# Performance work log

Hardware: AMD Instinct MI355X
Metric: run time of the kernel (lower is better)

## Reference

```python
import jax, jax.numpy as jnp
import numpy as np

N, E, F, D, EH, G, L, NG = 50000, 800000, 32, 32, 96, 128, 3, 500


def setup_inputs() -> dict:
    key = jax.random.key(0)
    ks = iter(jax.random.split(key, 32))
    w = lambda shape: jax.random.normal(next(ks), shape, dtype=jnp.float32) * 0.05
    inp = {
        "node_features": jax.random.normal(next(ks), (N, F), dtype=jnp.float32),
        "enc_W": w((F, D)), "enc_b": w((D,)),
        "msg_W1": w((L, 2 * D, EH)), "msg_b1": w((L, EH)),
        "msg_W2": w((L, EH, EH)), "msg_b2": w((L, EH)),
        "rmsg_W1": w((L, 2 * D, EH)), "rmsg_b1": w((L, EH)),
        "rmsg_W2": w((L, EH, EH)), "rmsg_b2": w((L, EH)),
        "gru_Wih": w((L, 3 * D, EH)), "gru_Whh": w((L, 3 * D, D)),
        "gru_bih": w((L, 3 * D)), "gru_bhh": w((L, 3 * D)),
        "agg_W1": w((D, 2 * G)), "agg_b1": w((2 * G,)),
        "agg_W2": w((G, G)), "agg_b2": w((G,)),
        "from_idx": jax.random.randint(next(ks), (E,), 0, N),
        "to_idx": jax.random.randint(next(ks), (E,), 0, N),
        "graph_idx": jnp.sort(jax.random.randint(next(ks), (N,), 0, NG)),
        "n_graphs": NG,
    }
    return inp


def _mlp(x, W1, b1, W2, b2):
    # Linear -> ReLU -> Linear (message net)
    return jax.nn.relu(x @ W1 + b1) @ W2 + b2


def _gru_step(x, h, Wih, Whh, bih, bhh):
    # torch nn.GRU single-step, gate order r, z, n
    gi = x @ Wih.T + bih  # [n, 3D]
    gh = h @ Whh.T + bhh  # [n, 3D]
    ir, iz, inn = jnp.split(gi, 3, axis=-1)
    hr, hz, hn = jnp.split(gh, 3, axis=-1)
    r = jax.nn.sigmoid(ir + hr)
    z = jax.nn.sigmoid(iz + hz)
    n = jnp.tanh(inn + r * hn)
    return (1.0 - z) * n + z * h


def _forward(node_features, enc_W, enc_b, msg_W1, msg_b1, msg_W2, msg_b2,
             rmsg_W1, rmsg_b1, rmsg_W2, rmsg_b2, gru_Wih, gru_Whh, gru_bih, gru_bhh,
             agg_W1, agg_b1, agg_W2, agg_b2, from_idx, to_idx, graph_idx, n_graphs):
    # GraphEncoder: single Linear
    h = node_features @ enc_W + enc_b  # [N, D]
    n_nodes = h.shape[0]
    n_layers = msg_W1.shape[0]
    for l in range(n_layers):  # small fixed layer count
        fs = h[from_idx]  # [E, D] gather
        ts = h[to_idx]    # [E, D] gather
        # forward-direction messages: gather -> concat -> MLP -> scatter_add to to_idx
        m = _mlp(jnp.concatenate([fs, ts], axis=-1), msg_W1[l], msg_b1[l], msg_W2[l], msg_b2[l])
        agg = jax.ops.segment_sum(m, to_idx, num_segments=n_nodes)
        # reverse direction: roles of from/to swapped, scatter to from_idx
        mr = _mlp(jnp.concatenate([ts, fs], axis=-1), rmsg_W1[l], rmsg_b1[l], rmsg_W2[l], rmsg_b2[l])
        agg = agg + jax.ops.segment_sum(mr, from_idx, num_segments=n_nodes)
        # node update via GRU (aggregated messages as input, node states as hidden)
        h = _gru_step(agg, h, gru_Wih[l], gru_Whh[l], gru_bih[l], gru_bhh[l])
    # GraphAggregator: gated node transform + scatter_add by graph, then Linear
    g = h @ agg_W1 + agg_b1  # [N, 2G]
    gdim = agg_W2.shape[0]
    gated = jax.nn.sigmoid(g[:, :gdim]) * g[:, gdim:]
    graph_states = jax.ops.segment_sum(gated, graph_idx, num_segments=n_graphs)  # [n_graphs, G]
    return graph_states @ agg_W2 + agg_b2


def reference(node_features, enc_W, enc_b, msg_W1, msg_b1, msg_W2, msg_b2,
              rmsg_W1, rmsg_b1, rmsg_W2, rmsg_b2, gru_Wih, gru_Whh, gru_bih, gru_bhh,
              agg_W1, agg_b1, agg_W2, agg_b2, from_idx, to_idx, graph_idx, n_graphs):
    return _forward(node_features, enc_W, enc_b, msg_W1, msg_b1, msg_W2, msg_b2,
                    rmsg_W1, rmsg_b1, rmsg_W2, rmsg_b2, gru_Wih, gru_Whh, gru_bih, gru_bhh,
                    agg_W1, agg_b1, agg_W2, agg_b2, from_idx, to_idx, graph_idx, n_graphs)
```

## Files before the change

### kernel.cpp

```cpp
#include <hip/hip_runtime.h>

#define SB 512

typedef __attribute__((ext_vector_type(8))) short short8;
typedef __attribute__((ext_vector_type(4))) float f32x4;

__device__ inline unsigned short f2bf(float f) {
    unsigned u = __float_as_uint(f);
    unsigned r = (u + 0x7fffu + ((u >> 16) & 1u)) >> 16;
    return (unsigned short)r;
}
__device__ inline unsigned pack2bf(float x, float y) {
    return (unsigned)f2bf(x) | ((unsigned)f2bf(y) << 16);
}

__global__ void count_rank_kernel(const int* __restrict__ from_idx, const int* __restrict__ to_idx,
                                  int* __restrict__ cnt_to, int* __restrict__ cnt_from,
                                  int* __restrict__ rank_to, int* __restrict__ rank_from, int E) {
    int e = blockIdx.x * blockDim.x + threadIdx.x;
    if (e >= E) return;
    int f = from_idx[e], t = to_idx[e];
    rank_to[e] = atomicAdd(&cnt_to[t], 1);
    rank_from[e] = atomicAdd(&cnt_from[f], 1);
}

__global__ void __launch_bounds__(SB) scanA_kernel(const int* __restrict__ cnt_to,
                                                   const int* __restrict__ cnt_from,
                                                   int* __restrict__ bsum, int nblk, int N) {
    const int* cnt = blockIdx.y ? cnt_from : cnt_to;
    __shared__ int s[SB];
    int tid = threadIdx.x;
    int i = blockIdx.x * SB + tid;
    s[tid] = (i < N) ? cnt[i] : 0;
    __syncthreads();
    for (int d = SB / 2; d > 0; d >>= 1) {
        if (tid < d) s[tid] += s[tid + d];
        __syncthreads();
    }
    if (tid == 0) bsum[blockIdx.y * nblk + blockIdx.x] = s[0];
}

__global__ void scanB_kernel(int* __restrict__ bsum, int* __restrict__ bbase,
                             int* __restrict__ off_to, int* __restrict__ off_from,
                             int nblk, int N) {
    int tid = threadIdx.x;
    if (tid < 2) {
        const int* bs = bsum + tid * nblk;
        int* bb = bbase + tid * nblk;
        int run = 0;
        for (int i = 0; i < nblk; ++i) { bb[i] = run; run += bs[i]; }
        if (tid == 0) off_to[N] = run; else off_from[N] = run;
    }
}

__global__ void __launch_bounds__(SB) scanC_kernel(const int* __restrict__ cnt_to,
                                                   const int* __restrict__ cnt_from,
                                                   const int* __restrict__ bbase,
                                                   int* __restrict__ off_to, int* __restrict__ off_from,
                                                   int nblk, int N) {
    const int* cnt = blockIdx.y ? cnt_from : cnt_to;
    int* off = blockIdx.y ? off_from : off_to;
    __shared__ int s[SB];
    int tid = threadIdx.x;
    int i = blockIdx.x * SB + tid;
    int v = (i < N) ? cnt[i] : 0;
    s[tid] = v;
    __syncthreads();
    for (int d = 1; d < SB; d <<= 1) {
        int t = s[tid];
        int add = (tid >= d) ? s[tid - d] : 0;
        __syncthreads();
        s[tid] = t + add;
        __syncthreads();
    }
    if (i < N) off[i] = s[tid] - v + bbase[blockIdx.y * nblk + blockIdx.x];
}

__global__ void fill_kernel(const int* __restrict__ from_idx, const int* __restrict__ to_idx,
                            const int* __restrict__ off_to, const int* __restrict__ off_from,
                            const int* __restrict__ rank_to, const int* __restrict__ rank_from,
                            int* __restrict__ list_to, int* __restrict__ list_from, int E) {
    int e = blockIdx.x * blockDim.x + threadIdx.x;
    if (e >= E) return;
    int f = from_idx[e], t = to_idx[e];
    list_to[off_to[t] + rank_to[e]] = f;
    list_from[off_from[f] + rank_from[e]] = t;
}

__global__ void compose_kernel(const float* __restrict__ W2, const float* __restrict__ rW2,
                               const float* __restrict__ Wih,
                               const float* __restrict__ b2, const float* __restrict__ rb2,
                               float* __restrict__ M1, float* __restrict__ M2,
                               float* __restrict__ v12) {
    int l = blockIdx.x / 97, j = blockIdx.x % 97;
    int k = threadIdx.x;
    const float* wih = Wih + l * 9216 + k * 96;
    if (j < 96) {
        const float* w2  = W2 + l * 9216 + j * 96;
        const float* rw2 = rW2 + l * 9216 + j * 96;
        float a1 = 0.f, a2 = 0.f;
        for (int m = 0; m < 96; ++m) {
            float wv = wih[m];
            a1 = fmaf(w2[m], wv, a1);
            a2 = fmaf(rw2[m], wv, a2);
        }
        M1[l * 9216 + j * 96 + k] = a1;
        M2[l * 9216 + j * 96 + k] = a2;
    } else {
        const float* bb = b2 + l * 96;
        const float* rbb = rb2 + l * 96;
        float a1 = 0.f, a2 = 0.f;
        for (int m = 0; m < 96; ++m) {
            float wv = wih[m];
            a1 = fmaf(bb[m], wv, a1);
            a2 = fmaf(rbb[m], wv, a2);
        }
        v12[l * 192 + k] = a1;
        v12[l * 192 + 96 + k] = a2;
    }
}

__global__ void repack_kernel(const float* __restrict__ M1, const float* __restrict__ M2,
                              const float* __restrict__ Whh,
                              const float* __restrict__ W1f, const float* __restrict__ W1r,
                              unsigned* __restrict__ M1bc, unsigned* __restrict__ M2bc,
                              unsigned* __restrict__ Whhbc, unsigned* __restrict__ W1bc) {
    int idx = blockIdx.x * 256 + threadIdx.x;
    if (idx < 13824) {
        int l = idx / 4608, r = idx % 4608, c = r / 48, wd = r % 48;
        const float* src = M1 + l * 9216;
        M1bc[idx] = pack2bf(src[(2 * wd) * 96 + c], src[(2 * wd + 1) * 96 + c]);
    } else if (idx < 27648) {
        int j = idx - 13824;
        int l = j / 4608, r = j % 4608, c = r / 48, wd = r % 48;
        const float* src = M2 + l * 9216;
        M2bc[j] = pack2bf(src[(2 * wd) * 96 + c], src[(2 * wd + 1) * 96 + c]);
    } else if (idx < 32256) {
        int j = idx - 27648;
        int l = j / 1536, r = j % 1536, c = r / 16, wd = r % 16;
        const float* src = Whh + l * 3072 + c * 32;
        Whhbc[j] = pack2bf(src[2 * wd], src[2 * wd + 1]);
    } else if (idx < 32256 + 18432) {
        int j = idx - 32256;
        int l = j / 6144, r = j % 6144, C = r / 16, wd = r % 16;
        const float* src; int col, rb;
        if (C < 96)       { src = W1f + l * 6144; col = C;       rb = 0;  }
        else if (C < 192) { src = W1f + l * 6144; col = C - 96;  rb = 32; }
        else if (C < 288) { src = W1r + l * 6144; col = C - 192; rb = 0;  }
        else              { src = W1r + l * 6144; col = C - 288; rb = 32; }
        W1bc[j] = pack2bf(src[(rb + 2 * wd) * 96 + col], src[(rb + 2 * wd + 1) * 96 + col]);
    }
}

__global__ void __launch_bounds__(256) enc_gemm(const float* __restrict__ IN,
                                                const float* __restrict__ W, const float* __restrict__ bias,
                                                float* __restrict__ OUT, unsigned short* __restrict__ hb16, int N) {
    __shared__ float tile[64][33];
    int n0 = blockIdx.x * 64, tid = threadIdx.x;
    for (int idx = tid; idx < 64 * 32; idx += 256) {
        int r = idx >> 5, c = idx & 31;
        int n = n0 + r;
        tile[r][c] = (n < N) ? IN[(long)n * 32 + c] : 0.f;
    }
    __syncthreads();
    int lane = tid & 63;
    int w = __builtin_amdgcn_readfirstlane(tid >> 6);
    float acc[8] = {0};
    const float* Wp = W + w * 8;
#pragma unroll 4
    for (int j = 0; j < 32; ++j) {
        float a = tile[lane][j];
#pragma unroll
        for (int c = 0; c < 8; ++c) acc[c] = fmaf(a, Wp[j * 32 + c], acc[c]);
    }
    int n = n0 + lane;
    if (n >= N) return;
    float* outp = OUT + (long)n * 32 + w * 8;
    unsigned short* bp = hb16 + (long)n * 32 + w * 8;
#pragma unroll
    for (int c = 0; c < 8; ++c) {
        float v = acc[c] + bias[w * 8 + c];
        outp[c] = v;
        bp[c] = f2bf(v);
    }
}

__global__ void __launch_bounds__(512) proj_mfma(
    const unsigned* __restrict__ hb, const unsigned* __restrict__ W1bc,
    const float* __restrict__ b1f, const float* __restrict__ b1r,
    unsigned short* __restrict__ PaF16, unsigned short* __restrict__ PbF16,
    unsigned short* __restrict__ PaR16, unsigned short* __restrict__ PbR16, int N)
{
    int tid = threadIdx.x;
    int lane = tid & 63;
    int w = __builtin_amdgcn_readfirstlane(tid >> 6);
    int nt = w >> 1, cg = w & 1;
    int kgrp = lane >> 4, l15 = lane & 15;
    int ntile = blockIdx.x * 64 + nt * 16;
    int arow = ntile + l15;
    long arc = (arow < N) ? arow : (N - 1);
    short8 a = *(const short8*)(hb + arc * 16 + kgrp * 4);

    unsigned short* Pa16 = cg ? PaR16 : PaF16;
    unsigned short* Pb16 = cg ? PbR16 : PbF16;
    const float* b1 = cg ? b1r : b1f;

    f32x4 acc[12];
#pragma unroll
    for (int ct = 0; ct < 12; ++ct) {
        int col = cg * 192 + ct * 16 + l15;
        short8 b = *(const short8*)(W1bc + (long)col * 16 + kgrp * 4);
        acc[ct] = __builtin_amdgcn_mfma_f32_16x16x32_bf16(a, b, (f32x4){0.f,0.f,0.f,0.f}, 0, 0, 0);
    }
    int nbase = ntile + kgrp * 4;
#pragma unroll
    for (int ct = 0; ct < 6; ++ct) {
        int col = ct * 16 + l15;
#pragma unroll
        for (int i = 0; i < 4; ++i) {
            int n = nbase + i;
            if (n < N) Pa16[(long)n * 96 + col] = f2bf(acc[ct][i]);
        }
    }
#pragma unroll
    for (int ct = 6; ct < 12; ++ct) {
        int col = (ct - 6) * 16 + l15;
        float bv = b1[col];
#pragma unroll
        for (int i = 0; i < 4; ++i) {
            int n = nbase + i;
            if (n < N) Pb16[(long)n * 96 + col] = f2bf(acc[ct][i] + bv);
        }
    }
}

__global__ void __launch_bounds__(256) agg_bf16(
    const int* __restrict__ offF, const int* __restrict__ listF,
    const int* __restrict__ offR, const int* __restrict__ listR,
    const unsigned* __restrict__ PaF, const unsigned* __restrict__ PaR,
    const unsigned short* __restrict__ PbF16, const unsigned short* __restrict__ PbR16,
    unsigned* __restrict__ AFb, unsigned* __restrict__ ARb, int N)
{
    const int* off; const int* list; const unsigned* Pa; const unsigned short* Pb16; unsigned* AB;
    if (blockIdx.y == 0) { off = offF; list = listF; Pa = PaF; Pb16 = PbF16; AB = AFb; }
    else                 { off = offR; list = listR; Pa = PaR; Pb16 = PbR16; AB = ARb; }
    int n = __builtin_amdgcn_readfirstlane((blockIdx.x * 256 + threadIdx.x) >> 6);
    int lane = threadIdx.x & 63;
    if (n >= N) return;
    int li = (lane < 48) ? lane : 47;
    bool act = lane < 48;
    float sx = 0.f, sy = 0.f;
    if (act) {
        unsigned s = *(const unsigned*)(Pb16 + (long)n * 96 + 2 * li);
        sx = __uint_as_float(s << 16);
        sy = __uint_as_float(s & 0xffff0000u);
    }
    float a0 = 0.f, a1 = 0.f;
    int beg = off[n], end = off[n + 1];
    if (end > beg) {
        int nb = (end - beg + 7) >> 3;
        for (int b = 0; b < nb; ++b) {
            int base = beg + b * 8;
            unsigned u[8]; float m[8];
#pragma unroll
            for (int q = 0; q < 8; ++q) {
                int idx = base + q;
                bool v = idx < end;
                int src = list[v ? idx : end - 1];
                u[q] = Pa[(long)src * 48 + li];
                m[q] = v ? 1.f : 0.f;
            }
#pragma unroll
            for (int q = 0; q < 8; ++q) {
                a0 += m[q] * fmaxf(__uint_as_float(u[q] << 16) + sx, 0.f);
                a1 += m[q] * fmaxf(__uint_as_float(u[q] & 0xffff0000u) + sy, 0.f);
            }
        }
    }
    if (act) AB[(long)n * 48 + li] = pack2bf(a0, a1);
}

__global__ void __launch_bounds__(512) gru3_kernel(
    const unsigned* __restrict__ AFb, const unsigned* __restrict__ ARb,
    const unsigned* __restrict__ M1bc, const unsigned* __restrict__ M2bc,
    const unsigned* __restrict__ Whhbc,
    const float* __restrict__ v12,
    const int* __restrict__ offF, const int* __restrict__ offR,
    const float* __restrict__ h, const unsigned* __restrict__ hb,
    const float* __restrict__ bih, const float* __restrict__ bhh,
    float* __restrict__ hout, unsigned short* __restrict__ hbout, int N)
{
    int tid = threadIdx.x;
    int lane = tid & 63;
    int w = __builtin_amdgcn_readfirstlane(tid >> 6);
    int nt = w >> 1, cg = w & 1;
    int kgrp = lane >> 4;
    int c = cg * 16 + (lane & 15);
    int ntile = blockIdx.x * 64 + nt * 16;
    int arow = ntile + (lane & 15);
    long arc = (arow < N) ? arow : (N - 1);

    f32x4 acc[3]; f32x4 gh[3];
#pragma unroll
    for (int g = 0; g < 3; ++g) { acc[g] = (f32x4){0.f,0.f,0.f,0.f}; gh[g] = (f32x4){0.f,0.f,0.f,0.f}; }

    const unsigned* afp = AFb + arc * 48 + kgrp * 4;
    const unsigned* arp = ARb + arc * 48 + kgrp * 4;
#pragma unroll
    for (int k0 = 0; k0 < 3; ++k0) {
        short8 a = *(const short8*)(afp + k0 * 16);
#pragma unroll
        for (int g = 0; g < 3; ++g) {
            int col = g * 32 + c;
            short8 b = *(const short8*)(M1bc + (long)col * 48 + k0 * 16 + kgrp * 4);
            acc[g] = __builtin_amdgcn_mfma_f32_16x16x32_bf16(a, b, acc[g], 0, 0, 0);
        }
    }
#pragma unroll
    for (int k0 = 0; k0 < 3; ++k0) {
        short8 a = *(const short8*)(arp + k0 * 16);
#pragma unroll
        for (int g = 0; g < 3; ++g) {
            int col = g * 32 + c;
            short8 b = *(const short8*)(M2bc + (long)col * 48 + k0 * 16 + kgrp * 4);
            acc[g] = __builtin_amdgcn_mfma_f32_16x16x32_bf16(a, b, acc[g], 0, 0, 0);
        }
    }
    {
        short8 ha = *(const short8*)(hb + arc * 16 + kgrp * 4);
#pragma unroll
        for (int g = 0; g < 3; ++g) {
            int col = g * 32 + c;
            short8 b = *(const short8*)(Whhbc + (long)col * 16 + kgrp * 4);
            gh[g] = __builtin_amdgcn_mfma_f32_16x16x32_bf16(ha, b, gh[g], 0, 0, 0);
        }
    }

    float v1r[3], v2r[3], bihv[3], bhhv[3];
#pragma unroll
    for (int g = 0; g < 3; ++g) {
        int col = g * 32 + c;
        v1r[g] = v12[col]; v2r[g] = v12[96 + col];
        bihv[g] = bih[col]; bhhv[g] = bhh[col];
    }
    int nbase = ntile + kgrp * 4;
#pragma unroll
    for (int i = 0; i < 4; ++i) {
        int n = nbase + i;
        if (n < N) {
            float dF = (float)(offF[n + 1] - offF[n]);
            float dR = (float)(offR[n + 1] - offR[n]);
            float gir = acc[0][i] + dF * v1r[0] + dR * v2r[0] + bihv[0];
            float giz = acc[1][i] + dF * v1r[1] + dR * v2r[1] + bihv[1];
            float gin = acc[2][i] + dF * v1r[2] + dR * v2r[2] + bihv[2];
            float r = 1.f / (1.f + __expf(-(gir + gh[0][i] + bhhv[0])));
            float z = 1.f / (1.f + __expf(-(giz + gh[1][i] + bhhv[1])));
            float nn = tanhf(gin + r * (gh[2][i] + bhhv[2]));
            float hv = h[(long)n * 32 + c];
            float vout = (1.f - z) * nn + z * hv;
            hout[(long)n * 32 + c] = vout;
            hbout[(long)n * 32 + c] = f2bf(vout);
        }
    }
}

__global__ void __launch_bounds__(128) graph_agg(const float* __restrict__ h, const float* __restrict__ W1,
                          const float* __restrict__ b1, const int* __restrict__ gidx,
                          float* __restrict__ gs, int N, int chunk) {
    int k = threadIdx.x;
    int n_start = blockIdx.x * chunk;
    if (n_start >= N) return;
    int n_end = min(n_start + chunk, N);
    float w1[32], w2[32];
#pragma unroll
    for (int j = 0; j < 32; ++j) {
        w1[j] = W1[j * 256 + k];
        w2[j] = W1[j * 256 + 128 + k];
    }
    float bb1 = b1[k], bb2 = b1[128 + k];
    float acc = 0.f;
    int cur = gidx[n_start];
    for (int n = n_start; n < n_end; ++n) {
        int g = gidx[n];
        if (g != cur) { atomicAdd(&gs[cur * 128 + k], acc); acc = 0.f; cur = g; }
        float g1 = bb1, g2 = bb2;
#pragma unroll
        for (int j = 0; j < 32; ++j) {
            float hv = h[(long)n * 32 + j];
            g1 = fmaf(hv, w1[j], g1);
            g2 = fmaf(hv, w2[j], g2);
        }
        acc += (1.f / (1.f + __expf(-g1))) * g2;
    }
    atomicAdd(&gs[cur * 128 + k], acc);
}

__global__ void final_gemm(const float* __restrict__ gs, const float* __restrict__ W,
                           const float* __restrict__ b, float* __restrict__ out) {
    int g = blockIdx.x, k = threadIdx.x;
    float a = b[k];
#pragma unroll 8
    for (int j = 0; j < 128; ++j) a = fmaf(gs[g * 128 + j], W[j * 128 + k], a);
    out[g * 128 + k] = a;
}

extern "C" void kernel_launch(void* const* d_in, const int* in_sizes, int n_in,
                              void* d_out, int out_size, void* d_ws, size_t ws_size,
                              hipStream_t stream) {
    const float* node_features = (const float*)d_in[0];
    const float* enc_W  = (const float*)d_in[1];
    const float* enc_b  = (const float*)d_in[2];
    const float* msg_W1 = (const float*)d_in[3];
    const float* msg_b1 = (const float*)d_in[4];
    const float* msg_W2 = (const float*)d_in[5];
    const float* msg_b2 = (const float*)d_in[6];
    const float* rmsg_W1 = (const float*)d_in[7];
    const float* rmsg_b1 = (const float*)d_in[8];
    const float* rmsg_W2 = (const float*)d_in[9];
    const float* rmsg_b2 = (const float*)d_in[10];
    const float* gru_Wih = (const float*)d_in[11];
    const float* gru_Whh = (const float*)d_in[12];
    const float* gru_bih = (const float*)d_in[13];
    const float* gru_bhh = (const float*)d_in[14];
    const float* agg_W1 = (const float*)d_in[15];
    const float* agg_b1 = (const float*)d_in[16];
    const float* agg_W2 = (const float*)d_in[17];
    const float* agg_b2 = (const float*)d_in[18];
    const int* from_idx = (const int*)d_in[19];
    const int* to_idx   = (const int*)d_in[20];
    const int* graph_idx = (const int*)d_in[21];

    const int N = in_sizes[0] / 32;
    const int E = in_sizes[19];
    const int NG = out_size / 128;
    float* out = (float*)d_out;

    char* ws = (char*)d_ws;
    auto alloc = [&](size_t b) { void* p = (void*)ws; ws += (b + 255) & ~(size_t)255; return p; };
    int* cnt_to   = (int*)alloc((size_t)N * 4);
    int* cnt_from = (int*)alloc((size_t)N * 4);
    int* off_to   = (int*)alloc((size_t)(N + 1) * 4);
    int* off_from = (int*)alloc((size_t)(N + 1) * 4);
    int* list_to  = (int*)alloc((size_t)E * 4);
    int* list_from= (int*)alloc((size_t)E * 4);
    float* h0  = (float*)alloc((size_t)N * 32 * 4);
    float* h1  = (float*)alloc((size_t)N * 32 * 4);
    unsigned* PaF = (unsigned*)alloc((size_t)N * 48 * 4);
    unsigned* PaR = (unsigned*)alloc((size_t)N * 48 * 4);
    unsigned short* PbF16 = (unsigned short*)alloc((size_t)N * 96 * 2);
    unsigned short* PbR16 = (unsigned short*)alloc((size_t)N * 96 * 2);
    unsigned* AFb = (unsigned*)alloc((size_t)N * 48 * 4);
    unsigned* ARb = (unsigned*)alloc((size_t)N * 48 * 4);
    unsigned* hb0 = (unsigned*)alloc((size_t)N * 16 * 4);
    unsigned* hb1 = (unsigned*)alloc((size_t)N * 16 * 4);
    float* M1   = (float*)alloc((size_t)3 * 96 * 96 * 4);
    float* M2   = (float*)alloc((size_t)3 * 96 * 96 * 4);
    float* v12  = (float*)alloc((size_t)3 * 192 * 4);
    unsigned* M1bc = (unsigned*)alloc((size_t)13824 * 4);
    unsigned* M2bc = (unsigned*)alloc((size_t)13824 * 4);
    unsigned* Whhbc = (unsigned*)alloc((size_t)4608 * 4);
    unsigned* W1bc  = (unsigned*)alloc((size_t)18432 * 4);
    float* gs   = (float*)alloc((size_t)NG * 128 * 4);
    const int nblk = (N + SB - 1) / SB;
    int* bsum  = (int*)alloc((size_t)2 * nblk * 4);
    int* bbase = (int*)alloc((size_t)2 * nblk * 4);
    int* rank_to   = (int*)PaF;
    int* rank_from = (int*)PaR;

    hipMemsetAsync(cnt_to, 0, (size_t)N * 4, stream);
    hipMemsetAsync(cnt_from, 0, (size_t)N * 4, stream);
    hipMemsetAsync(gs, 0, (size_t)NG * 128 * 4, stream);

    int gE = (E + 255) / 256;
    count_rank_kernel<<<gE, 256, 0, stream>>>(from_idx, to_idx, cnt_to, cnt_from, rank_to, rank_from, E);
    dim3 gScan(nblk, 2);
    scanA_kernel<<<gScan, SB, 0, stream>>>(cnt_to, cnt_from, bsum, nblk, N);
    scanB_kernel<<<1, 64, 0, stream>>>(bsum, bbase, off_to, off_from, nblk, N);
    scanC_kernel<<<gScan, SB, 0, stream>>>(cnt_to, cnt_from, bbase, off_to, off_from, nblk, N);
    fill_kernel<<<gE, 256, 0, stream>>>(from_idx, to_idx, off_to, off_from, rank_to, rank_from,
                                        list_to, list_from, E);

    compose_kernel<<<3 * 97, 96, 0, stream>>>(msg_W2, rmsg_W2, gru_Wih, msg_b2, rmsg_b2, M1, M2, v12);
    repack_kernel<<<(32256 + 18432 + 255) / 256, 256, 0, stream>>>(M1, M2, gru_Whh, msg_W1, rmsg_W1,
                                                                   M1bc, M2bc, Whhbc, W1bc);

    int gN64 = (N + 63) / 64;
    enc_gemm<<<gN64, 256, 0, stream>>>(node_features, enc_W, enc_b, h0, (unsigned short*)hb0, N);

    float* hcur = h0; float* hnext = h1;
    unsigned* hbcur = hb0; unsigned* hbnext = hb1;
    dim3 gAgg((N + 3) / 4, 2);
    for (int l = 0; l < 3; ++l) {
        proj_mfma<<<gN64, 512, 0, stream>>>(hbcur, W1bc + l * 6144,
                                            msg_b1 + l * 96, rmsg_b1 + l * 96,
                                            (unsigned short*)PaF, PbF16, (unsigned short*)PaR, PbR16, N);
        agg_bf16<<<gAgg, 256, 0, stream>>>(off_to, list_to, off_from, list_from,
                                           PaF, PaR, PbF16, PbR16, AFb, ARb, N);
        gru3_kernel<<<gN64, 512, 0, stream>>>(AFb, ARb, M1bc + l * 4608, M2bc + l * 4608,
                                              Whhbc + l * 1536, v12 + l * 192,
                                              off_to, off_from, hcur, hbcur,
                                              gru_bih + l * 96, gru_bhh + l * 96, hnext,
                                              (unsigned short*)hbnext, N);
        float* t = hcur; hcur = hnext; hnext = t;
        unsigned* tb = hbcur; hbcur = hbnext; hbnext = tb;
    }

    const int chunk = 32;
    graph_agg<<<(N + chunk - 1) / chunk, 128, 0, stream>>>(hcur, agg_W1, agg_b1, graph_idx, gs, N, chunk);
    final_gemm<<<NG, 128, 0, stream>>>(gs, agg_W2, agg_b2, out);
}
```

Measured before the change: 431.2 us.

## Fuse next-layer message projection into GRU kernel epilogue

Measured after the change: 427.6 us. Within noise of the previous version (-0.8%).

```diff
diff --git a/kernel.cpp b/kernel.cpp
--- a/kernel.cpp
+++ b/kernel.cpp
@@ -280,7 +280,8 @@
     if (act) AB[(long)n * 48 + li] = pack2bf(a0, a1);
 }
 
-__global__ void __launch_bounds__(512) gru3_kernel(
+template <int DO_PROJ>
+__global__ void __launch_bounds__(512) gru3_proj(
     const unsigned* __restrict__ AFb, const unsigned* __restrict__ ARb,
     const unsigned* __restrict__ M1bc, const unsigned* __restrict__ M2bc,
     const unsigned* __restrict__ Whhbc,
@@ -288,16 +289,20 @@
     const int* __restrict__ offF, const int* __restrict__ offR,
     const float* __restrict__ h, const unsigned* __restrict__ hb,
     const float* __restrict__ bih, const float* __restrict__ bhh,
-    float* __restrict__ hout, unsigned short* __restrict__ hbout, int N)
+    float* __restrict__ hout, unsigned short* __restrict__ hbout,
+    const unsigned* __restrict__ W1bc, const float* __restrict__ b1f, const float* __restrict__ b1r,
+    unsigned short* __restrict__ PaF16, unsigned short* __restrict__ PbF16,
+    unsigned short* __restrict__ PaR16, unsigned short* __restrict__ PbR16, int N)
 {
+    __shared__ unsigned short hs[64 * 40];
     int tid = threadIdx.x;
     int lane = tid & 63;
     int w = __builtin_amdgcn_readfirstlane(tid >> 6);
     int nt = w >> 1, cg = w & 1;
-    int kgrp = lane >> 4;
-    int c = cg * 16 + (lane & 15);
+    int kgrp = lane >> 4, l15 = lane & 15;
+    int c = cg * 16 + l15;
     int ntile = blockIdx.x * 64 + nt * 16;
-    int arow = ntile + (lane & 15);
+    int arow = ntile + l15;
     long arc = (arow < N) ? arow : (N - 1);
 
     f32x4 acc[3]; f32x4 gh[3];
@@ -359,7 +364,43 @@
             float hv = h[(long)n * 32 + c];
             float vout = (1.f - z) * nn + z * hv;
             hout[(long)n * 32 + c] = vout;
-            hbout[(long)n * 32 + c] = f2bf(vout);
+            unsigned short v16 = f2bf(vout);
+            hbout[(long)n * 32 + c] = v16;
+            if (DO_PROJ) hs[(nt * 16 + kgrp * 4 + i) * 40 + c] = v16;
+        }
+    }
+    if (DO_PROJ) {
+        __syncthreads();
+        const unsigned* hsw = (const unsigned*)hs;
+        short8 a = *(const short8*)(hsw + (nt * 16 + l15) * 20 + kgrp * 4);
+        unsigned short* Pa16 = cg ? PaR16 : PaF16;
+        unsigned short* Pb16 = cg ? PbR16 : PbF16;
+        const float* b1 = cg ? b1r : b1f;
+        f32x4 pacc[12];
+#pragma unroll
+        for (int ct = 0; ct < 12; ++ct) {
+            int col = cg * 192 + ct * 16 + l15;
+            short8 b = *(const short8*)(W1bc + (long)col * 16 + kgrp * 4);
+            pacc[ct] = __builtin_amdgcn_mfma_f32_16x16x32_bf16(a, b, (f32x4){0.f,0.f,0.f,0.f}, 0, 0, 0);
+        }
+#pragma unroll
+        for (int ct = 0; ct < 6; ++ct) {
+            int col = ct * 16 + l15;
+#pragma unroll
+            for (int i = 0; i < 4; ++i) {
+                int n = nbase + i;
+                if (n < N) Pa16[(long)n * 96 + col] = f2bf(pacc[ct][i]);
+            }
+        }
+#pragma unroll
+        for (int ct = 6; ct < 12; ++ct) {
+            int col = (ct - 6) * 16 + l15;
+            float bv = b1[col];
+#pragma unroll
+            for (int i = 0; i < 4; ++i) {
+                int n = nbase + i;
+                if (n < N) Pb16[(long)n * 96 + col] = f2bf(pacc[ct][i] + bv);
+            }
         }
     }
 }
@@ -437,8 +478,9 @@
 
     char* ws = (char*)d_ws;
     auto alloc = [&](size_t b) { void* p = (void*)ws; ws += (b + 255) & ~(size_t)255; return p; };
-    int* cnt_to   = (int*)alloc((size_t)N * 4);
-    int* cnt_from = (int*)alloc((size_t)N * 4);
+    int* cnt2     = (int*)alloc((size_t)2 * N * 4);
+    int* cnt_to   = cnt2;
+    int* cnt_from = cnt2 + N;
     int* off_to   = (int*)alloc((size_t)(N + 1) * 4);
     int* off_from = (int*)alloc((size_t)(N + 1) * 4);
     int* list_to  = (int*)alloc((size_t)E * 4);
@@ -467,8 +509,7 @@
     int* rank_to   = (int*)PaF;
     int* rank_from = (int*)PaR;
 
-    hipMemsetAsync(cnt_to, 0, (size_t)N * 4, stream);
-    hipMemsetAsync(cnt_from, 0, (size_t)N * 4, stream);
+    hipMemsetAsync(cnt2, 0, (size_t)2 * N * 4, stream);
     hipMemsetAsync(gs, 0, (size_t)NG * 128 * 4, stream);
 
     int gE = (E + 255) / 256;
@@ -487,20 +528,35 @@
     int gN64 = (N + 63) / 64;
     enc_gemm<<<gN64, 256, 0, stream>>>(node_features, enc_W, enc_b, h0, (unsigned short*)hb0, N);
 
+    proj_mfma<<<gN64, 512, 0, stream>>>(hb0, W1bc,
+                                        msg_b1, rmsg_b1,
+                                        (unsigned short*)PaF, PbF16, (unsigned short*)PaR, PbR16, N);
+
     float* hcur = h0; float* hnext = h1;
     unsigned* hbcur = hb0; unsigned* hbnext = hb1;
     dim3 gAgg((N + 3) / 4, 2);
     for (int l = 0; l < 3; ++l) {
-        proj_mfma<<<gN64, 512, 0, stream>>>(hbcur, W1bc + l * 6144,
-                                            msg_b1 + l * 96, rmsg_b1 + l * 96,
-                                            (unsigned short*)PaF, PbF16, (unsigned short*)PaR, PbR16, N);
         agg_bf16<<<gAgg, 256, 0, stream>>>(off_to, list_to, off_from, list_from,
                                            PaF, PaR, PbF16, PbR16, AFb, ARb, N);
-        gru3_kernel<<<gN64, 512, 0, stream>>>(AFb, ARb, M1bc + l * 4608, M2bc + l * 4608,
-                                              Whhbc + l * 1536, v12 + l * 192,
-                                              off_to, off_from, hcur, hbcur,
-                                              gru_bih + l * 96, gru_bhh + l * 96, hnext,
-                                              (unsigned short*)hbnext, N);
+        if (l < 2) {
+            gru3_proj<1><<<gN64, 512, 0, stream>>>(AFb, ARb, M1bc + l * 4608, M2bc + l * 4608,
+                                                   Whhbc + l * 1536, v12 + l * 192,
+                                                   off_to, off_from, hcur, hbcur,
+                                                   gru_bih + l * 96, gru_bhh + l * 96, hnext,
+                                                   (unsigned short*)hbnext,
+                                                   W1bc + (l + 1) * 6144, msg_b1 + (l + 1) * 96,
+                                                   rmsg_b1 + (l + 1) * 96,
+                                                   (unsigned short*)PaF, PbF16,
+                                                   (unsigned short*)PaR, PbR16, N);
+        } else {
+            gru3_proj<0><<<gN64, 512, 0, stream>>>(AFb, ARb, M1bc + l * 4608, M2bc + l * 4608,
+                                                   Whhbc + l * 1536, v12 + l * 192,
+                                                   off_to, off_from, hcur, hbcur,
+                                                   gru_bih + l * 96, gru_bhh + l * 96, hnext,
+                                                   (unsigned short*)hbnext,
+                                                   nullptr, nullptr, nullptr,
+                                                   nullptr, nullptr, nullptr, nullptr, N);
+        }
         float* t = hcur; hcur = hnext; hnext = t;
         unsigned* tb = hbcur; hbcur = hbnext; hbnext = tb;
     }
```
